# Optimization experiments

Hardware: AMD Instinct MI355X
Metric: run time of the kernel (lower is better)

The kernel has to match this reference:

```python
import jax, jax.numpy as jnp
import numpy as np

N = 50000
F = 128
E = 800000
HOP = 3
ALPHA = 0.2  # leaky relu slope


def setup_inputs() -> dict:
    key = jax.random.key(0)
    ks = jax.random.split(key, 6)
    x = jax.random.normal(ks[0], (N, F), dtype=jnp.float32)
    h0 = jax.random.normal(ks[1], (N, F), dtype=jnp.float32)
    edge_index = jax.random.randint(ks[2], (2, E), 0, N, dtype=jnp.int32)
    edge_weight = jax.random.uniform(ks[3], (E,), dtype=jnp.float32)
    # xavier-uniform-ish params
    lim_w = float(np.sqrt(6.0 / (F + F)))
    W_att = jax.random.uniform(ks[4], (F, F), dtype=jnp.float32, minval=-lim_w, maxval=lim_w)
    lim_a = 1.414 * float(np.sqrt(6.0 / (2 * F + 1)))
    a = jax.random.uniform(ks[5], (2 * F, 1), dtype=jnp.float32, minval=-lim_a, maxval=lim_a)
    temp = jnp.zeros((4,), dtype=jnp.float32)
    return {"x": x, "h0": h0, "edge_index": edge_index, "edge_weight": edge_weight,
            "W_att": W_att, "a": a, "temp": temp}


def _segment_softmax(e, rows, num_segments):
    m = jax.ops.segment_max(e, rows, num_segments=num_segments)
    m = jnp.where(jnp.isfinite(m), m, 0.0)  # guard empty rows
    ex = jnp.exp(e - m[rows])
    s = jax.ops.segment_sum(ex, rows, num_segments=num_segments)
    s = jnp.where(s > 0, s, 1.0)
    return ex / s[rows]


def reference(x, h0, edge_index, edge_weight, W_att, a, temp):
    rows, cols = edge_index[0], edge_index[1]
    # --- attention (edge-wise, never materializing dense NxN e) ---
    feat = x @ W_att                       # [N, F]
    f1 = (feat @ a[:F]).squeeze(-1)        # [N]
    f2 = (feat @ a[F:]).squeeze(-1)        # [N]
    e = f1[rows] + f2[cols]                # e[i,j] at edges
    e = jnp.where(e > 0, e, ALPHA * e)     # leaky relu
    att = _segment_softmax(e, rows, N)     # sparse row softmax values
    P = 0.5 * att
    # --- lifting bases ---
    coe = jax.nn.sigmoid(temp)
    rowsum = jax.ops.segment_sum(edge_weight * P, rows, num_segments=N)  # [N]
    update = x
    feat_prime = None
    for step in range(HOP):
        # sparse mm: U @ update
        update = jax.ops.segment_sum(att[:, None] * update[cols], rows, num_segments=N)
        feat_even = coe[0] * x + update
        feat_odd = update - feat_even * rowsum[:, None]
        feat_prime = feat_odd if step == 0 else coe[2] * feat_prime + (1.0 - coe[2]) * feat_odd
    return feat_prime
```

## Files before the change

kernel.cpp:

```cpp
#include <hip/hip_runtime.h>
#include <hip/hip_fp16.h>

#define NN 50000
#define FF 128
#define EE 800000
#define ALPHA 0.2f
#define ESHIFT 4.0f

#define NBINS 196
#define CAPB 5120
#define EPB 2048
#define NWIN 784
#define WCAP 1600

__global__ void k_w(const float* __restrict__ W, const float* __restrict__ a,
                    float* __restrict__ w12) {
    int k = threadIdx.x;
    float s1 = 0.f, s2 = 0.f;
    const float* wr = W + k * FF;
    for (int j = 0; j < FF; ++j) {
        float w = wr[j];
        s1 += w * a[j];
        s2 += w * a[FF + j];
    }
    w12[k] = s1;
    w12[FF + k] = s2;
}

__global__ void k_f(const float* __restrict__ x, const float* __restrict__ w12,
                    float* __restrict__ f1, float* __restrict__ f2,
                    __half* __restrict__ xh) {
    int gid = blockIdx.x * blockDim.x + threadIdx.x;
    int node = gid >> 6;
    int lane = threadIdx.x & 63;
    if (node >= NN) return;
    float2 xv = ((const float2*)(x + (size_t)node * FF))[lane];
    ((__half2*)(xh + (size_t)node * FF))[lane] = __float22half2_rn(xv);
    float2 w1 = ((const float2*)w12)[lane];
    float2 w2 = ((const float2*)(w12 + FF))[lane];
    float s1 = xv.x * w1.x + xv.y * w1.y;
    float s2 = xv.x * w2.x + xv.y * w2.y;
#pragma unroll
    for (int o = 32; o > 0; o >>= 1) {
        s1 += __shfl_down(s1, o);
        s2 += __shfl_down(s2, o);
    }
    if (lane == 0) { f1[node] = s1; f2[node] = s2; }
}

__global__ void k_bin(const int* __restrict__ rows, const int* __restrict__ cols,
                      const float* __restrict__ ew, const float* __restrict__ f1,
                      const float* __restrict__ f2, int* __restrict__ bin_fill,
                      int2* __restrict__ binbuf) {
    __shared__ int cnt[NBINS];
    __shared__ int gbase[NBINS];
    int tid = threadIdx.x;
    if (tid < NBINS) cnt[tid] = 0;
    __syncthreads();
    int e0 = blockIdx.x * EPB;
    int rk[8], bn[8], rc[8], pay[8];
    bool vl[8];
#pragma unroll
    for (int k = 0; k < 8; ++k) {
        int e = e0 + k * 256 + tid;
        vl[k] = e < EE;
        if (vl[k]) {
            int r = rows[e], c = cols[e];
            float v = f1[r] + f2[c];
            v = v > 0.f ? v : ALPHA * v;
            float ex = __expf(v - ESHIFT);
            union { int i; __half2 h; } p;
            p.h = __floats2half2_rn(ex, ew[e] * ex);
            pay[k] = p.i;
            rc[k] = (r << 16) | c;
            bn[k] = r >> 8;
            rk[k] = atomicAdd(&cnt[bn[k]], 1);
        }
    }
    __syncthreads();
    if (tid < NBINS) {
        int c0 = cnt[tid];
        gbase[tid] = c0 ? atomicAdd(&bin_fill[tid], c0) : 0;
    }
    __syncthreads();
#pragma unroll
    for (int k = 0; k < 8; ++k) {
        if (vl[k]) {
            int pos = gbase[bn[k]] + rk[k];
            if (pos < CAPB) binbuf[(size_t)bn[k] * CAPB + pos] = make_int2(rc[k], pay[k]);
        }
    }
}

__global__ void k_csr(const int* __restrict__ bin_fill, const int2* __restrict__ binbuf,
                      int2* __restrict__ csr, int2* __restrict__ rowinfo) {
    __shared__ int lfill[64];
    __shared__ int pbase[65];
    __shared__ int cursor[64];
    int tid = threadIdx.x;
    int w = blockIdx.x;
    int bin = w >> 2, q = w & 3;
    int cnt = bin_fill[bin];
    if (cnt > CAPB) cnt = CAPB;
    if (tid < 64) lfill[tid] = 0;
    __syncthreads();
    const int2* bb = binbuf + (size_t)bin * CAPB;
    for (int i = tid; i < cnt; i += 256) {
        int rl = (bb[i].x >> 16) & 0xFF;
        if ((rl >> 6) == q) atomicAdd(&lfill[rl & 63], 1);
    }
    __syncthreads();
    if (tid < 64) {
        int pc = (lfill[tid] + 1) & ~1;
        int s = pc;
#pragma unroll
        for (int o = 1; o < 64; o <<= 1) {
            int t = __shfl_up(s, o);
            if (tid >= o) s += t;
        }
        pbase[tid + 1] = s;
        if (tid == 0) pbase[0] = 0;
    }
    __syncthreads();
    int wbase = w * WCAP;
    if (tid < 64) cursor[tid] = wbase + pbase[tid];
    __syncthreads();
    for (int i = tid; i < cnt; i += 256) {
        int2 e = bb[i];
        int rl = (e.x >> 16) & 0xFF;
        if ((rl >> 6) == q) {
            int p = atomicAdd(&cursor[rl & 63], 1);
            csr[p] = make_int2(e.x & 0xFFFF, e.y);
        }
    }
    __syncthreads();
    if (tid < 64) {
        int r = (bin << 8) + (q << 6) + tid;
        if (r < NN) {
            int beg = wbase + pbase[tid];
            int dreal = lfill[tid];
            int dpad = (dreal + 1) & ~1;
            if (dreal & 1) csr[beg + dreal] = make_int2(0, 0);
            rowinfo[r] = make_int2(beg, dpad);
        }
    }
}

__global__ void k_hop(const float* __restrict__ x, const __half* __restrict__ uin,
                      __half* __restrict__ uout, const int2* __restrict__ rowinfo,
                      const int2* __restrict__ csr, const float* __restrict__ temp,
                      __half* __restrict__ S, float* __restrict__ out, int step) {
    int wave = threadIdx.x >> 6;
    int lane = threadIdx.x & 63;
    int r = __builtin_amdgcn_readfirstlane(blockIdx.x * 4 + wave);
    if (r >= NN) return;
    int2 ri = rowinfo[r];
    const unsigned long long* bk = (const unsigned long long*)(csr + ri.x);
    int d = ri.y;
    float ax = 0.f, ay = 0.f, se = 0.f, sw = 0.f;
    int j = 0;
    for (; j + 8 <= d; j += 8) {
        unsigned long long b[8];
        __half2 h[8];
#pragma unroll
        for (int t = 0; t < 8; ++t) b[t] = __builtin_nontemporal_load(bk + j + t);
#pragma unroll
        for (int t = 0; t < 8; ++t) {
            int col = (int)(unsigned)(b[t] & 0xFFFFFFFFull);
            h[t] = ((const __half2*)(uin + (size_t)col * FF))[lane];
        }
#pragma unroll
        for (int t = 0; t < 8; ++t) {
            union { unsigned u; __half2 h2; } p;
            p.u = (unsigned)(b[t] >> 32);
            float2 ee = __half22float2(p.h2);
            float2 u = __half22float2(h[t]);
            ax += ee.x * u.x;
            ay += ee.x * u.y;
            se += ee.x;
            sw += ee.y;
        }
    }
    for (; j < d; ++j) {
        unsigned long long b = __builtin_nontemporal_load(bk + j);
        int col = (int)(unsigned)(b & 0xFFFFFFFFull);
        __half2 hv = ((const __half2*)(uin + (size_t)col * FF))[lane];
        union { unsigned u; __half2 h2; } p;
        p.u = (unsigned)(b >> 32);
        float2 ee = __half22float2(p.h2);
        float2 u = __half22float2(hv);
        ax += ee.x * u.x;
        ay += ee.x * u.y;
        se += ee.x;
        sw += ee.y;
    }
    float inv = se > 0.f ? 1.f / se : 0.f;
    ax *= inv;
    ay *= inv;
    float c2 = 1.f / (1.f + __expf(-temp[2]));
    __half2* Sr = (__half2*)(S + (size_t)r * FF);
    if (step == 0) {
        ((__half2*)(uout + (size_t)r * FF))[lane] = __float22half2_rn(make_float2(ax, ay));
        float w0 = c2 * c2;
        Sr[lane] = __float22half2_rn(make_float2(w0 * ax, w0 * ay));
    } else if (step == 1) {
        ((__half2*)(uout + (size_t)r * FF))[lane] = __float22half2_rn(make_float2(ax, ay));
        float w1 = c2 * (1.f - c2);
        float2 sv = __half22float2(Sr[lane]);
        Sr[lane] = __float22half2_rn(make_float2(sv.x + w1 * ax, sv.y + w1 * ay));
    } else {
        float rs = 0.5f * sw * inv;
        float coe0 = 1.f / (1.f + __expf(-temp[0]));
        float w2 = 1.f - c2;
        float2 sv = __half22float2(Sr[lane]);
        float2 xv = ((const float2*)(x + (size_t)r * FF))[lane];
        float k1 = 1.f - rs;
        float k2 = coe0 * rs;
        ((float2*)(out + (size_t)r * FF))[lane] =
            make_float2(k1 * (sv.x + w2 * ax) - k2 * xv.x,
                        k1 * (sv.y + w2 * ay) - k2 * xv.y);
    }
}

extern "C" void kernel_launch(void* const* d_in, const int* in_sizes, int n_in,
                              void* d_out, int out_size, void* d_ws, size_t ws_size,
                              hipStream_t stream) {
    const float* x = (const float*)d_in[0];
    const int* eidx = (const int*)d_in[2];
    const int* rows = eidx;
    const int* cols = eidx + EE;
    const float* ew = (const float*)d_in[3];
    const float* W = (const float*)d_in[4];
    const float* a = (const float*)d_in[5];
    const float* temp = (const float*)d_in[6];
    float* out = (float*)d_out;

    float* ws = (float*)d_ws;
    int* bin_fill = (int*)ws;
    float* w12 = ws + 256;
    float* f1 = ws + 512;
    float* f2 = f1 + NN;
    int2* rowinfo = (int2*)(f2 + NN);
    int2* csr = rowinfo + NN;
    __half* xh = (__half*)(csr + (size_t)NWIN * WCAP);
    __half* uh0 = xh + (size_t)NN * FF;
    __half* Sb = uh0 + (size_t)NN * FF;
    int2* binbuf = (int2*)Sb;
    __half* uh1 = xh;

    hipMemsetAsync(bin_fill, 0, NBINS * sizeof(int), stream);

    k_w<<<1, 128, 0, stream>>>(W, a, w12);
    k_f<<<(NN + 3) / 4, 256, 0, stream>>>(x, w12, f1, f2, xh);
    k_bin<<<(EE + EPB - 1) / EPB, 256, 0, stream>>>(rows, cols, ew, f1, f2, bin_fill, binbuf);
    k_csr<<<NWIN, 256, 0, stream>>>(bin_fill, binbuf, csr, rowinfo);
    k_hop<<<(NN + 3) / 4, 256, 0, stream>>>(x, xh, uh0, rowinfo, csr, temp, Sb, out, 0);
    k_hop<<<(NN + 3) / 4, 256, 0, stream>>>(x, uh0, uh1, rowinfo, csr, temp, Sb, out, 1);
    k_hop<<<(NN + 3) / 4, 256, 0, stream>>>(x, uh1, nullptr, rowinfo, csr, temp, Sb, out, 2);
}
```

Before: 247.5 us.

## Split each row's edges across four 16-lane groups with 16-byte gathers

The hop kernel now splits each wave into four 16-lane subgroups. Each subgroup handles a different edge and gathers a full 128-half feature row with 16-byte loads instead of 4-byte loads per lane, and the partial sums are combined with cross-lane xor shuffles. CSR rows are padded to a multiple of 4 with zero-weight edges so every subgroup has an edge on each step. The aim is fewer, wider memory transactions and more edges in flight per wave. The cost is extra padding edges, a shuffle reduction, more registers, and only a quarter of the lanes doing the output writes.

```diff
diff --git a/kernel.cpp b/kernel.cpp
--- a/kernel.cpp
+++ b/kernel.cpp
@@ -111,7 +111,7 @@
     }
     __syncthreads();
     if (tid < 64) {
-        int pc = (lfill[tid] + 1) & ~1;
+        int pc = (lfill[tid] + 3) & ~3;
         int s = pc;
 #pragma unroll
         for (int o = 1; o < 64; o <<= 1) {
@@ -139,8 +139,8 @@
         if (r < NN) {
             int beg = wbase + pbase[tid];
             int dreal = lfill[tid];
-            int dpad = (dreal + 1) & ~1;
-            if (dreal & 1) csr[beg + dreal] = make_int2(0, 0);
+            int dpad = (dreal + 3) & ~3;
+            for (int t = dreal; t < dpad; ++t) csr[beg + t] = make_int2(0, 0);
             rowinfo[r] = make_int2(beg, dpad);
         }
     }
@@ -157,68 +157,119 @@
     int2 ri = rowinfo[r];
     const unsigned long long* bk = (const unsigned long long*)(csr + ri.x);
     int d = ri.y;
-    float ax = 0.f, ay = 0.f, se = 0.f, sw = 0.f;
+    int s = lane >> 4;
+    int fl = lane & 15;
+    float ax[8];
+#pragma unroll
+    for (int k = 0; k < 8; ++k) ax[k] = 0.f;
+    float se = 0.f, sw = 0.f;
     int j = 0;
-    for (; j + 8 <= d; j += 8) {
-        unsigned long long b[8];
-        __half2 h[8];
-#pragma unroll
-        for (int t = 0; t < 8; ++t) b[t] = __builtin_nontemporal_load(bk + j + t);
-#pragma unroll
-        for (int t = 0; t < 8; ++t) {
-            int col = (int)(unsigned)(b[t] & 0xFFFFFFFFull);
-            h[t] = ((const __half2*)(uin + (size_t)col * FF))[lane];
-        }
-#pragma unroll
-        for (int t = 0; t < 8; ++t) {
+    for (; j + 16 <= d; j += 16) {
+        unsigned long long b[4];
+        uint4 h[4];
+#pragma unroll
+        for (int g = 0; g < 4; ++g)
+            b[g] = __builtin_nontemporal_load(bk + j + 4 * g + s);
+#pragma unroll
+        for (int g = 0; g < 4; ++g) {
+            int col = (int)(unsigned)(b[g] & 0xFFFFFFFFull);
+            h[g] = ((const uint4*)(uin + (size_t)col * FF))[fl];
+        }
+#pragma unroll
+        for (int g = 0; g < 4; ++g) {
             union { unsigned u; __half2 h2; } p;
-            p.u = (unsigned)(b[t] >> 32);
+            p.u = (unsigned)(b[g] >> 32);
             float2 ee = __half22float2(p.h2);
-            float2 u = __half22float2(h[t]);
-            ax += ee.x * u.x;
-            ay += ee.x * u.y;
             se += ee.x;
             sw += ee.y;
-        }
-    }
-    for (; j < d; ++j) {
-        unsigned long long b = __builtin_nontemporal_load(bk + j);
+            const __half2* hh = (const __half2*)&h[g];
+#pragma unroll
+            for (int t = 0; t < 4; ++t) {
+                float2 u2 = __half22float2(hh[t]);
+                ax[2 * t] += ee.x * u2.x;
+                ax[2 * t + 1] += ee.x * u2.y;
+            }
+        }
+    }
+    for (; j < d; j += 4) {
+        unsigned long long b = __builtin_nontemporal_load(bk + j + s);
         int col = (int)(unsigned)(b & 0xFFFFFFFFull);
-        __half2 hv = ((const __half2*)(uin + (size_t)col * FF))[lane];
+        uint4 h = ((const uint4*)(uin + (size_t)col * FF))[fl];
         union { unsigned u; __half2 h2; } p;
         p.u = (unsigned)(b >> 32);
         float2 ee = __half22float2(p.h2);
-        float2 u = __half22float2(hv);
-        ax += ee.x * u.x;
-        ay += ee.x * u.y;
         se += ee.x;
         sw += ee.y;
+        const __half2* hh = (const __half2*)&h;
+#pragma unroll
+        for (int t = 0; t < 4; ++t) {
+            float2 u2 = __half22float2(hh[t]);
+            ax[2 * t] += ee.x * u2.x;
+            ax[2 * t + 1] += ee.x * u2.y;
+        }
+    }
+#pragma unroll
+    for (int o = 16; o < 64; o <<= 1) {
+#pragma unroll
+        for (int k = 0; k < 8; ++k) ax[k] += __shfl_xor(ax[k], o);
+        se += __shfl_xor(se, o);
+        sw += __shfl_xor(sw, o);
     }
     float inv = se > 0.f ? 1.f / se : 0.f;
-    ax *= inv;
-    ay *= inv;
+#pragma unroll
+    for (int k = 0; k < 8; ++k) ax[k] *= inv;
     float c2 = 1.f / (1.f + __expf(-temp[2]));
-    __half2* Sr = (__half2*)(S + (size_t)r * FF);
+    uint4* Sr = (uint4*)(S + (size_t)r * FF);
     if (step == 0) {
-        ((__half2*)(uout + (size_t)r * FF))[lane] = __float22half2_rn(make_float2(ax, ay));
-        float w0 = c2 * c2;
-        Sr[lane] = __float22half2_rn(make_float2(w0 * ax, w0 * ay));
+        if (s == 0) {
+            union { uint4 u; __half2 h2[4]; } o1, o2;
+            float w0 = c2 * c2;
+#pragma unroll
+            for (int t = 0; t < 4; ++t) {
+                o1.h2[t] = __floats2half2_rn(ax[2 * t], ax[2 * t + 1]);
+                o2.h2[t] = __floats2half2_rn(w0 * ax[2 * t], w0 * ax[2 * t + 1]);
+            }
+            ((uint4*)(uout + (size_t)r * FF))[fl] = o1.u;
+            Sr[fl] = o2.u;
+        }
     } else if (step == 1) {
-        ((__half2*)(uout + (size_t)r * FF))[lane] = __float22half2_rn(make_float2(ax, ay));
-        float w1 = c2 * (1.f - c2);
-        float2 sv = __half22float2(Sr[lane]);
-        Sr[lane] = __float22half2_rn(make_float2(sv.x + w1 * ax, sv.y + w1 * ay));
+        if (s == 0) {
+            float w1 = c2 * (1.f - c2);
+            union { uint4 u; __half2 h2[4]; } o1, sv;
+            sv.u = Sr[fl];
+#pragma unroll
+            for (int t = 0; t < 4; ++t) {
+                o1.h2[t] = __floats2half2_rn(ax[2 * t], ax[2 * t + 1]);
+                float2 svf = __half22float2(sv.h2[t]);
+                sv.h2[t] = __floats2half2_rn(svf.x + w1 * ax[2 * t],
+                                             svf.y + w1 * ax[2 * t + 1]);
+            }
+            ((uint4*)(uout + (size_t)r * FF))[fl] = o1.u;
+            Sr[fl] = sv.u;
+        }
     } else {
-        float rs = 0.5f * sw * inv;
-        float coe0 = 1.f / (1.f + __expf(-temp[0]));
-        float w2 = 1.f - c2;
-        float2 sv = __half22float2(Sr[lane]);
-        float2 xv = ((const float2*)(x + (size_t)r * FF))[lane];
-        float k1 = 1.f - rs;
-        float k2 = coe0 * rs;
-        ((float2*)(out + (size_t)r * FF))[lane] =
-            make_float2(k1 * (sv.x + w2 * ax) - k2 * xv.x,
-                        k1 * (sv.y + w2 * ay) - k2 * xv.y);
+        if (s == 0) {
+            float rs = 0.5f * sw * inv;
+            float coe0 = 1.f / (1.f + __expf(-temp[0]));
+            float w2 = 1.f - c2;
+            float k1 = 1.f - rs, k2 = coe0 * rs;
+            union { uint4 u; __half2 h2[4]; } sv;
+            sv.u = Sr[fl];
+            const float4* xr = (const float4*)(x + (size_t)r * FF);
+            float4* orow = (float4*)(out + (size_t)r * FF);
+            float4 xv0 = xr[2 * fl], xv1 = xr[2 * fl + 1];
+            float res[8];
+#pragma unroll
+            for (int t = 0; t < 4; ++t) {
+                float2 svf = __half22float2(sv.h2[t]);
+                res[2 * t] = k1 * (svf.x + w2 * ax[2 * t]);
+                res[2 * t + 1] = k1 * (svf.y + w2 * ax[2 * t + 1]);
+            }
+            orow[2 * fl] = make_float4(res[0] - k2 * xv0.x, res[1] - k2 * xv0.y,
+                                       res[2] - k2 * xv0.z, res[3] - k2 * xv0.w);
+            orow[2 * fl + 1] = make_float4(res[4] - k2 * xv1.x, res[5] - k2 * xv1.y,
+                                           res[6] - k2 * xv1.z, res[7] - k2 * xv1.w);
+        }
     }
 }
 
```

Measured after the change: 248.9 us. No clear change (+0.6%).

## Slab-partition feature matrix so each hop pass gathers cache-resident 16-wide slices

Applied to the files above, without the earlier changes.

Feature vectors are stored as 8 column slabs of 16 halves per node, and the hop kernel is split across slabs so each launch slice gathers from a 1.6MB slab that can stay in cache instead of random full-row gathers. Each wave processes two rows at once, with 16 edges in parallel per row and 4 lanes per slab, then reduces with shuffles. The row-sum term is precomputed in the CSR build, which now pads rows to multiples of four. This adds 8x the CSR index reads per hop and more shuffle reductions in exchange for better gather locality.

```diff
diff --git a/kernel.cpp b/kernel.cpp
--- a/kernel.cpp
+++ b/kernel.cpp
@@ -12,6 +12,13 @@
 #define EPB 2048
 #define NWIN 784
 #define WCAP 1600
+#define NSL 8
+#define SLW 16
+#define BPS 2048
+#define WPS (BPS * 4)
+
+union H4 { uint2 u; __half2 h[2]; };
+union H2 { unsigned u; int i; __half2 h; };
 
 __global__ void k_w(const float* __restrict__ W, const float* __restrict__ a,
                     float* __restrict__ w12) {
@@ -35,7 +42,8 @@
     int lane = threadIdx.x & 63;
     if (node >= NN) return;
     float2 xv = ((const float2*)(x + (size_t)node * FF))[lane];
-    ((__half2*)(xh + (size_t)node * FF))[lane] = __float22half2_rn(xv);
+    int slab = lane >> 3, p = lane & 7;
+    ((__half2*)(xh + ((size_t)slab * NN + node) * SLW))[p] = __float22half2_rn(xv);
     float2 w1 = ((const float2*)w12)[lane];
     float2 w2 = ((const float2*)(w12 + FF))[lane];
     float s1 = xv.x * w1.x + xv.y * w1.y;
@@ -69,7 +77,7 @@
             float v = f1[r] + f2[c];
             v = v > 0.f ? v : ALPHA * v;
             float ex = __expf(v - ESHIFT);
-            union { int i; __half2 h; } p;
+            H2 p;
             p.h = __floats2half2_rn(ex, ew[e] * ex);
             pay[k] = p.i;
             rc[k] = (r << 16) | c;
@@ -93,7 +101,8 @@
 }
 
 __global__ void k_csr(const int* __restrict__ bin_fill, const int2* __restrict__ binbuf,
-                      int2* __restrict__ csr, int2* __restrict__ rowinfo) {
+                      int2* __restrict__ csr, int2* __restrict__ rowinfo,
+                      float* __restrict__ rs) {
     __shared__ int lfill[64];
     __shared__ int pbase[65];
     __shared__ int cursor[64];
@@ -111,7 +120,7 @@
     }
     __syncthreads();
     if (tid < 64) {
-        int pc = (lfill[tid] + 1) & ~1;
+        int pc = (lfill[tid] + 3) & ~3;
         int s = pc;
 #pragma unroll
         for (int o = 1; o < 64; o <<= 1) {
@@ -139,86 +148,143 @@
         if (r < NN) {
             int beg = wbase + pbase[tid];
             int dreal = lfill[tid];
-            int dpad = (dreal + 1) & ~1;
-            if (dreal & 1) csr[beg + dreal] = make_int2(0, 0);
+            int dpad = (dreal + 3) & ~3;
+            float se = 0.f, sw = 0.f;
+            for (int i = 0; i < dreal; ++i) {
+                H2 pu;
+                pu.i = csr[beg + i].y;
+                float2 f = __half22float2(pu.h);
+                se += f.x;
+                sw += f.y;
+            }
+            rs[r] = se > 0.f ? 0.5f * sw / se : 0.f;
+            for (int t = dreal; t < dpad; ++t) csr[beg + t] = make_int2(0, 0);
             rowinfo[r] = make_int2(beg, dpad);
         }
     }
 }
 
-__global__ void k_hop(const float* __restrict__ x, const __half* __restrict__ uin,
-                      __half* __restrict__ uout, const int2* __restrict__ rowinfo,
-                      const int2* __restrict__ csr, const float* __restrict__ temp,
-                      __half* __restrict__ S, float* __restrict__ out, int step) {
-    int wave = threadIdx.x >> 6;
-    int lane = threadIdx.x & 63;
-    int r = __builtin_amdgcn_readfirstlane(blockIdx.x * 4 + wave);
-    if (r >= NN) return;
-    int2 ri = rowinfo[r];
-    const unsigned long long* bk = (const unsigned long long*)(csr + ri.x);
-    int d = ri.y;
-    float ax = 0.f, ay = 0.f, se = 0.f, sw = 0.f;
-    int j = 0;
-    for (; j + 8 <= d; j += 8) {
-        unsigned long long b[8];
-        __half2 h[8];
-#pragma unroll
-        for (int t = 0; t < 8; ++t) b[t] = __builtin_nontemporal_load(bk + j + t);
-#pragma unroll
-        for (int t = 0; t < 8; ++t) {
-            int col = (int)(unsigned)(b[t] & 0xFFFFFFFFull);
-            h[t] = ((const __half2*)(uin + (size_t)col * FF))[lane];
-        }
-#pragma unroll
-        for (int t = 0; t < 8; ++t) {
-            union { unsigned u; __half2 h2; } p;
-            p.u = (unsigned)(b[t] >> 32);
-            float2 ee = __half22float2(p.h2);
-            float2 u = __half22float2(h[t]);
-            ax += ee.x * u.x;
-            ay += ee.x * u.y;
-            se += ee.x;
-            sw += ee.y;
-        }
-    }
-    for (; j < d; ++j) {
-        unsigned long long b = __builtin_nontemporal_load(bk + j);
-        int col = (int)(unsigned)(b & 0xFFFFFFFFull);
-        __half2 hv = ((const __half2*)(uin + (size_t)col * FF))[lane];
-        union { unsigned u; __half2 h2; } p;
-        p.u = (unsigned)(b >> 32);
-        float2 ee = __half22float2(p.h2);
-        float2 u = __half22float2(hv);
-        ax += ee.x * u.x;
-        ay += ee.x * u.y;
-        se += ee.x;
-        sw += ee.y;
-    }
+__device__ __forceinline__ void emit_row(
+    int step, int r, int sl, int fc, float a0, float a1, float a2, float a3, float se,
+    __half* __restrict__ uout_s, __half* __restrict__ S_s, const float* __restrict__ rs,
+    const float* __restrict__ x, float* __restrict__ out,
+    float w0, float w1c, float w2c, float coe0)
+{
     float inv = se > 0.f ? 1.f / se : 0.f;
-    ax *= inv;
-    ay *= inv;
+    a0 *= inv; a1 *= inv; a2 *= inv; a3 *= inv;
+    size_t pos = (size_t)r * SLW;
+    if (step == 0) {
+        H4 o1;
+        o1.h[0] = __floats2half2_rn(a0, a1);
+        o1.h[1] = __floats2half2_rn(a2, a3);
+        ((uint2*)(uout_s + pos))[fc] = o1.u;
+        H4 o2;
+        o2.h[0] = __floats2half2_rn(w0 * a0, w0 * a1);
+        o2.h[1] = __floats2half2_rn(w0 * a2, w0 * a3);
+        ((uint2*)(S_s + pos))[fc] = o2.u;
+    } else if (step == 1) {
+        H4 o1;
+        o1.h[0] = __floats2half2_rn(a0, a1);
+        o1.h[1] = __floats2half2_rn(a2, a3);
+        ((uint2*)(uout_s + pos))[fc] = o1.u;
+        H4 sv;
+        sv.u = ((const uint2*)(S_s + pos))[fc];
+        float2 s0 = __half22float2(sv.h[0]);
+        float2 s1 = __half22float2(sv.h[1]);
+        H4 sp;
+        sp.h[0] = __floats2half2_rn(s0.x + w1c * a0, s0.y + w1c * a1);
+        sp.h[1] = __floats2half2_rn(s1.x + w1c * a2, s1.y + w1c * a3);
+        ((uint2*)(S_s + pos))[fc] = sp.u;
+    } else {
+        float rsv = rs[r];
+        float k1 = 1.f - rsv, k2 = coe0 * rsv;
+        H4 sv;
+        sv.u = ((const uint2*)(S_s + pos))[fc];
+        float2 s0 = __half22float2(sv.h[0]);
+        float2 s1 = __half22float2(sv.h[1]);
+        float4 xv = ((const float4*)(x + (size_t)r * FF + sl * SLW))[fc];
+        float4 res;
+        res.x = k1 * (s0.x + w2c * a0) - k2 * xv.x;
+        res.y = k1 * (s0.y + w2c * a1) - k2 * xv.y;
+        res.z = k1 * (s1.x + w2c * a2) - k2 * xv.z;
+        res.w = k1 * (s1.y + w2c * a3) - k2 * xv.w;
+        ((float4*)(out + (size_t)r * FF + sl * SLW))[fc] = res;
+    }
+}
+
+__global__ __launch_bounds__(256) void k_hop(
+    const float* __restrict__ x, const __half* __restrict__ uin,
+    __half* __restrict__ uout, const int2* __restrict__ rowinfo,
+    const int2* __restrict__ csr, const float* __restrict__ temp,
+    const float* __restrict__ rs, __half* __restrict__ S,
+    float* __restrict__ out, int step)
+{
+    int wave = threadIdx.x >> 6, lane = threadIdx.x & 63;
+    int sl = blockIdx.x >> 11;
+    int wid = ((blockIdx.x & (BPS - 1)) << 2) + wave;
+    int slot = lane >> 2, fc = lane & 3;
+    const __half* uin_s = uin + (size_t)sl * NN * SLW;
+    __half* uout_s = uout + (size_t)sl * NN * SLW;
+    __half* S_s = S + (size_t)sl * NN * SLW;
     float c2 = 1.f / (1.f + __expf(-temp[2]));
-    __half2* Sr = (__half2*)(S + (size_t)r * FF);
-    if (step == 0) {
-        ((__half2*)(uout + (size_t)r * FF))[lane] = __float22half2_rn(make_float2(ax, ay));
-        float w0 = c2 * c2;
-        Sr[lane] = __float22half2_rn(make_float2(w0 * ax, w0 * ay));
-    } else if (step == 1) {
-        ((__half2*)(uout + (size_t)r * FF))[lane] = __float22half2_rn(make_float2(ax, ay));
-        float w1 = c2 * (1.f - c2);
-        float2 sv = __half22float2(Sr[lane]);
-        Sr[lane] = __float22half2_rn(make_float2(sv.x + w1 * ax, sv.y + w1 * ay));
-    } else {
-        float rs = 0.5f * sw * inv;
-        float coe0 = 1.f / (1.f + __expf(-temp[0]));
-        float w2 = 1.f - c2;
-        float2 sv = __half22float2(Sr[lane]);
-        float2 xv = ((const float2*)(x + (size_t)r * FF))[lane];
-        float k1 = 1.f - rs;
-        float k2 = coe0 * rs;
-        ((float2*)(out + (size_t)r * FF))[lane] =
-            make_float2(k1 * (sv.x + w2 * ax) - k2 * xv.x,
-                        k1 * (sv.y + w2 * ay) - k2 * xv.y);
+    float coe0 = 1.f / (1.f + __expf(-temp[0]));
+    float w0 = c2 * c2, w1c = c2 * (1.f - c2), w2c = 1.f - c2;
+    for (int r0 = wid; r0 < NN; r0 += WPS * 2) {
+        int rr1 = r0 + WPS;
+        int2 ri0 = rowinfo[r0];
+        int beg0 = ri0.x, d0 = ri0.y;
+        int beg1 = 0, d1 = 0;
+        if (rr1 < NN) { int2 ri1 = rowinfo[rr1]; beg1 = ri1.x; d1 = ri1.y; }
+        const unsigned long long* bk0 = (const unsigned long long*)(csr + beg0);
+        const unsigned long long* bk1 = (const unsigned long long*)(csr + beg1);
+        float a00 = 0.f, a01 = 0.f, a02 = 0.f, a03 = 0.f, se0 = 0.f;
+        float a10 = 0.f, a11 = 0.f, a12 = 0.f, a13 = 0.f, se1 = 0.f;
+        int dmax = d0 > d1 ? d0 : d1;
+        for (int j = slot; j < dmax; j += 16) {
+            unsigned long long b0 = 0, b1 = 0;
+            if (j < d0) b0 = __builtin_nontemporal_load(bk0 + j);
+            if (j < d1) b1 = __builtin_nontemporal_load(bk1 + j);
+            H4 v0, v1;
+            v0.u = make_uint2(0, 0);
+            v1.u = make_uint2(0, 0);
+            if (j < d0) v0.u = ((const uint2*)(uin_s + (size_t)(b0 & 0xFFFF) * SLW))[fc];
+            if (j < d1) v1.u = ((const uint2*)(uin_s + (size_t)(b1 & 0xFFFF) * SLW))[fc];
+            if (j < d0) {
+                H2 p0;
+                p0.u = (unsigned)(b0 >> 32);
+                float2 ee = __half22float2(p0.h);
+                float ex = ee.x;
+                float2 g0 = __half22float2(v0.h[0]);
+                float2 g1 = __half22float2(v0.h[1]);
+                se0 += ex;
+                a00 += ex * g0.x; a01 += ex * g0.y; a02 += ex * g1.x; a03 += ex * g1.y;
+            }
+            if (j < d1) {
+                H2 p1;
+                p1.u = (unsigned)(b1 >> 32);
+                float2 ee = __half22float2(p1.h);
+                float ex = ee.x;
+                float2 g0 = __half22float2(v1.h[0]);
+                float2 g1 = __half22float2(v1.h[1]);
+                se1 += ex;
+                a10 += ex * g0.x; a11 += ex * g0.y; a12 += ex * g1.x; a13 += ex * g1.y;
+            }
+        }
+#pragma unroll
+        for (int o = 4; o < 64; o <<= 1) {
+            a00 += __shfl_xor(a00, o); a01 += __shfl_xor(a01, o);
+            a02 += __shfl_xor(a02, o); a03 += __shfl_xor(a03, o);
+            a10 += __shfl_xor(a10, o); a11 += __shfl_xor(a11, o);
+            a12 += __shfl_xor(a12, o); a13 += __shfl_xor(a13, o);
+            se0 += __shfl_xor(se0, o); se1 += __shfl_xor(se1, o);
+        }
+        if (slot == 0) {
+            emit_row(step, r0, sl, fc, a00, a01, a02, a03, se0,
+                     uout_s, S_s, rs, x, out, w0, w1c, w2c, coe0);
+            if (rr1 < NN)
+                emit_row(step, rr1, sl, fc, a10, a11, a12, a13, se1,
+                         uout_s, S_s, rs, x, out, w0, w1c, w2c, coe0);
+        }
     }
 }
 
@@ -240,21 +306,22 @@
     float* w12 = ws + 256;
     float* f1 = ws + 512;
     float* f2 = f1 + NN;
-    int2* rowinfo = (int2*)(f2 + NN);
+    float* rs = f2 + NN;
+    int2* rowinfo = (int2*)(rs + NN);
     int2* csr = rowinfo + NN;
     __half* xh = (__half*)(csr + (size_t)NWIN * WCAP);
-    __half* uh0 = xh + (size_t)NN * FF;
-    __half* Sb = uh0 + (size_t)NN * FF;
+    __half* uh0 = xh + (size_t)NSL * NN * SLW;
+    __half* Sb = uh0 + (size_t)NSL * NN * SLW;
     int2* binbuf = (int2*)Sb;
     __half* uh1 = xh;
 
-    hipMemsetAsync(bin_fill, 0, NBINS * sizeof(int), stream);
+    (void)hipMemsetAsync(bin_fill, 0, NBINS * sizeof(int), stream);
 
     k_w<<<1, 128, 0, stream>>>(W, a, w12);
     k_f<<<(NN + 3) / 4, 256, 0, stream>>>(x, w12, f1, f2, xh);
     k_bin<<<(EE + EPB - 1) / EPB, 256, 0, stream>>>(rows, cols, ew, f1, f2, bin_fill, binbuf);
-    k_csr<<<NWIN, 256, 0, stream>>>(bin_fill, binbuf, csr, rowinfo);
-    k_hop<<<(NN + 3) / 4, 256, 0, stream>>>(x, xh, uh0, rowinfo, csr, temp, Sb, out, 0);
-    k_hop<<<(NN + 3) / 4, 256, 0, stream>>>(x, uh0, uh1, rowinfo, csr, temp, Sb, out, 1);
-    k_hop<<<(NN + 3) / 4, 256, 0, stream>>>(x, uh1, nullptr, rowinfo, csr, temp, Sb, out, 2);
-}
+    k_csr<<<NWIN, 256, 0, stream>>>(bin_fill, binbuf, csr, rowinfo, rs);
+    k_hop<<<NSL * BPS, 256, 0, stream>>>(x, xh, uh0, rowinfo, csr, temp, rs, Sb, out, 0);
+    k_hop<<<NSL * BPS, 256, 0, stream>>>(x, uh0, uh1, rowinfo, csr, temp, rs, Sb, out, 1);
+    k_hop<<<NSL * BPS, 256, 0, stream>>>(x, uh1, uh0, rowinfo, csr, temp, rs, Sb, out, 2);
+}
```

Result: slower. 521.2 us (+110.6%).
